# Performance work log

Hardware: AMD Instinct MI355X
Metric: run time of the kernel (lower is better)

The kernel has to match this reference:

```python
import jax, jax.numpy as jnp
import numpy as np

DIM = 768
NUM_HEADS = 1
AGENT_NUM = 4
HEAD_DIM = DIM // NUM_HEADS
SCALE = HEAD_DIM ** -0.5
B, N = 128, 196


def setup_inputs() -> dict:
    key = jax.random.key(0)
    ks = jax.random.split(key, 12)
    s = 0.02
    return {
        "x": jax.random.normal(ks[0], (B, N, DIM), jnp.float32),
        "attn_1": jax.random.normal(ks[1], (B, NUM_HEADS, AGENT_NUM, N), jnp.float32),
        "attn_2": jax.random.normal(ks[2], (B, NUM_HEADS, AGENT_NUM, N), jnp.float32),
        "agent_tk1": jax.random.normal(ks[3], (B, NUM_HEADS, AGENT_NUM, HEAD_DIM), jnp.float32),
        "agent_tk2": jax.random.normal(ks[4], (B, NUM_HEADS, AGENT_NUM, HEAD_DIM), jnp.float32),
        "W_qkv": jax.random.normal(ks[5], (DIM, 3 * DIM), jnp.float32) * s,
        "W_pool1": jax.random.normal(ks[6], (DIM, DIM // 2), jnp.float32) * s,
        "b_pool1": jnp.zeros((DIM // 2,), jnp.float32),
        "W_pool2": jax.random.normal(ks[7], (DIM // 2, NUM_HEADS * AGENT_NUM * DIM), jnp.float32) * s,
        "b_pool2": jnp.zeros((NUM_HEADS * AGENT_NUM * DIM,), jnp.float32),
        "W_proj": jax.random.normal(ks[8], (DIM, DIM), jnp.float32) * s,
        "b_proj": jnp.zeros((DIM,), jnp.float32),
    }


def reference(x, attn_1, attn_2, agent_tk1, agent_tk2,
              W_qkv, W_pool1, b_pool1, W_pool2, b_pool2, W_proj, b_proj):
    b, n, c = x.shape
    # qkv projection: (b, n, 3c) -> q, k, v each (b, n, c)
    qkv = x @ W_qkv
    q, k, v = jnp.split(qkv, 3, axis=-1)

    # agent tokens via pooling MLP on q (exact-erf GELU like torch nn.GELU)
    pooled = jax.nn.gelu(q @ W_pool1 + b_pool1, approximate=False) @ W_pool2 + b_pool2
    # mean over tokens -> (b, num_heads*agent_num*dim) == (b, agent_num*dim) since num_heads==1
    agent_tokens = pooled.mean(axis=1).reshape(b, AGENT_NUM, NUM_HEADS, HEAD_DIM)
    agent_tokens = agent_tokens.transpose(0, 2, 1, 3)  # (b, h, a, d)

    # split heads: (b, h, n, d)
    q = q.reshape(b, n, NUM_HEADS, HEAD_DIM).transpose(0, 2, 1, 3)
    k = k.reshape(b, n, NUM_HEADS, HEAD_DIM).transpose(0, 2, 1, 3)
    v = v.reshape(b, n, NUM_HEADS, HEAD_DIM).transpose(0, 2, 1, 3)

    # stage 1: agent attends to keys -> (b, h, a, n)
    agent_attn = jax.nn.softmax(jnp.einsum("bhad,bhnd->bhan", agent_tokens * SCALE, k), axis=-1)
    agent_rep = agent_attn

    # softmax blending with externally provided attn maps
    s = attn_1 + attn_2
    agent_attn = (agent_attn * jax.nn.softmax(s, axis=-1)
                  + agent_attn * jax.nn.softmax(s, axis=1)
                  + agent_attn) / 3.0

    agent_v = jnp.einsum("bhan,bhnd->bhad", agent_attn, v)  # (b, h, a, d)

    # blend agent tokens with external agent tokens
    t = agent_tk1 + agent_tk2
    agent_tokens = (agent_tokens * jax.nn.softmax(t, axis=-1)
                    + agent_tokens * jax.nn.softmax(t, axis=1)
                    + agent_tokens) / 3.0

    # stage 2: queries attend to agents -> (b, h, n, a)
    q_attn = jax.nn.softmax(jnp.einsum("bhnd,bhad->bhna", q * SCALE, agent_tokens), axis=-1)
    out = jnp.einsum("bhna,bhad->bhnd", q_attn, agent_v)  # (b, h, n, d)

    out = out.transpose(0, 2, 1, 3).reshape(b, n, c)
    out = out @ W_proj + b_proj
    return (out, agent_rep, agent_tokens)
```

## Files before the change

### kernel.cpp

```cpp
#include <hip/hip_runtime.h>
#include <hip/hip_bf16.h>
#include <math.h>

#define NB    128
#define NTOK  196
#define DIMC  768
#define AGN   4
#define SCALE_F 0.036084391824351614f

typedef __bf16  bf16x8  __attribute__((ext_vector_type(8)));
typedef float   f32x4   __attribute__((ext_vector_type(4)));
typedef unsigned short ushortx8 __attribute__((ext_vector_type(8)));
typedef unsigned short ushortx4 __attribute__((ext_vector_type(4)));

__device__ __forceinline__ unsigned short f2bf(float f) {
    union { float f; unsigned int u; } v; v.f = f;
    unsigned int r = v.u + 0x7fffu + ((v.u >> 16) & 1u);
    return (unsigned short)(r >> 16);
}
__device__ __forceinline__ float bf2f(unsigned short u) {
    union { unsigned int u; float f; } v; v.u = ((unsigned int)u) << 16;
    return v.f;
}
__device__ __forceinline__ void load_lds16(const void* g, void* l) {
    __builtin_amdgcn_global_load_lds(
        (const __attribute__((address_space(1))) unsigned int*)g,
        (__attribute__((address_space(3))) unsigned int*)l, 16, 0, 0);
}

template<int EPI>
__global__ __launch_bounds__(256) void gemm_bf16_k(
    const unsigned short* __restrict__ A, int lda,
    const unsigned short* __restrict__ Bt, int ldb,
    const float* __restrict__ bias,
    float* __restrict__ Cf, unsigned short* __restrict__ Cbf,
    int ldc, int K)
{
    __shared__ alignas(16) char lds[16384];

    const int nwg = gridDim.x * gridDim.y;
    const int id  = blockIdx.y * gridDim.x + blockIdx.x;
    const int q8  = nwg >> 3, r8 = nwg & 7;
    const int xcd = id & 7, off = id >> 3;
    const int nid = (xcd < r8 ? xcd * (q8 + 1) : r8 * (q8 + 1) + (xcd - r8) * q8) + off;
    const int bx = nid % gridDim.x, by = nid / gridDim.x;

    const int tid  = threadIdx.x;
    const int lane = tid & 63;
    const int wv   = tid >> 6;
    const int wr   = wv >> 1, wc = wv & 1;
    const int row0 = by * 128;
    const int col0 = bx * 128;

    const int c0 = wv * 2, c1 = wv * 2 + 1;
    const int srow = lane >> 2;
    const int skel = (lane & 3) << 3;
    const unsigned short* Ag0 = A  + (size_t)(row0 + c0*16 + srow) * lda + skel;
    const unsigned short* Ag1 = A  + (size_t)(row0 + c1*16 + srow) * lda + skel;
    const unsigned short* Bg0 = Bt + (size_t)(col0 + c0*16 + srow) * ldb + skel;
    const unsigned short* Bg1 = Bt + (size_t)(col0 + c1*16 + srow) * ldb + skel;
    char* lA0 = lds + c0 * 1024;
    char* lA1 = lds + c1 * 1024;
    char* lB0 = lds + 8192 + c0 * 1024;
    char* lB1 = lds + 8192 + c1 * 1024;

    f32x4 acc[4][4];
    #pragma unroll
    for (int m = 0; m < 4; m++)
        #pragma unroll
        for (int n = 0; n < 4; n++) acc[m][n] = (f32x4){0.f, 0.f, 0.f, 0.f};

    const int frow = lane & 15;
    const int kgrp = (lane >> 4) * 16;

    for (int bk = 0; bk < K; bk += 32) {
        __syncthreads();
        load_lds16(Ag0 + bk, lA0);
        load_lds16(Ag1 + bk, lA1);
        load_lds16(Bg0 + bk, lB0);
        load_lds16(Bg1 + bk, lB1);
        __syncthreads();

        bf16x8 af[4], bf[4];
        #pragma unroll
        for (int m = 0; m < 4; m++)
            af[m] = *(const bf16x8*)(lds + ((wr*64 + m*16 + frow) * 64 + kgrp));
        #pragma unroll
        for (int n = 0; n < 4; n++)
            bf[n] = *(const bf16x8*)(lds + 8192 + ((wc*64 + n*16 + frow) * 64 + kgrp));
        #pragma unroll
        for (int m = 0; m < 4; m++)
            #pragma unroll
            for (int n = 0; n < 4; n++)
                acc[m][n] = __builtin_amdgcn_mfma_f32_16x16x32_bf16(af[m], bf[n], acc[m][n], 0, 0, 0);
    }

    const int crow = (lane >> 4) << 2;
    #pragma unroll
    for (int n = 0; n < 4; n++) {
        const int col = col0 + wc*64 + n*16 + frow;
        const float bn = (EPI > 0) ? bias[col] : 0.f;
        #pragma unroll
        for (int m = 0; m < 4; m++) {
            #pragma unroll
            for (int r = 0; r < 4; r++) {
                const int row = row0 + wr*64 + m*16 + crow + r;
                float v = acc[m][n][r];
                if (EPI > 0) v += bn;
                if (EPI == 2) v = 0.5f * v * (1.f + erff(v * 0.7071067811865476f));
                if (EPI == 0) Cbf[(size_t)row * ldc + col] = f2bf(v);
                else          Cf [(size_t)row * ldc + col] = v;
            }
        }
    }
}

__global__ __launch_bounds__(256) void conv_k(const float* __restrict__ in,
                                              unsigned short* __restrict__ out)
{
    const size_t i = ((size_t)blockIdx.x * 256 + threadIdx.x) * 8;
    float4 v0 = *(const float4*)(in + i);
    float4 v1 = *(const float4*)(in + i + 4);
    ushortx8 o;
    o[0]=f2bf(v0.x); o[1]=f2bf(v0.y); o[2]=f2bf(v0.z); o[3]=f2bf(v0.w);
    o[4]=f2bf(v1.x); o[5]=f2bf(v1.y); o[6]=f2bf(v1.z); o[7]=f2bf(v1.w);
    *(ushortx8*)(out + i) = o;
}

__global__ __launch_bounds__(256) void tconv_k(const float* __restrict__ W,
                                               unsigned short* __restrict__ Wt,
                                               int K, int N)
{
    __shared__ float t[32][33];
    const int n0 = blockIdx.x * 32, k0 = blockIdx.y * 32;
    const int r = threadIdx.x >> 3;
    const int c = (threadIdx.x & 7) * 4;
    float4 v = *(const float4*)&W[(size_t)(k0 + r) * N + n0 + c];
    t[r][c] = v.x; t[r][c+1] = v.y; t[r][c+2] = v.z; t[r][c+3] = v.w;
    __syncthreads();
    ushortx4 o;
    o[0] = f2bf(t[c+0][r]); o[1] = f2bf(t[c+1][r]);
    o[2] = f2bf(t[c+2][r]); o[3] = f2bf(t[c+3][r]);
    *(ushortx4*)&Wt[(size_t)(n0 + r) * K + k0 + c] = o;
}

__global__ __launch_bounds__(128) void mean_k(const float* __restrict__ h1,
                                              float* __restrict__ mh)
{
    const int b = blockIdx.x;
    const int j = blockIdx.y * 128 + threadIdx.x;
    const float* p = h1 + (size_t)b * NTOK * 384 + j;
    float s0 = 0.f, s1 = 0.f, s2 = 0.f, s3 = 0.f;
    for (int n = 0; n < 196; n += 4) {
        s0 += p[(size_t)(n+0) * 384];
        s1 += p[(size_t)(n+1) * 384];
        s2 += p[(size_t)(n+2) * 384];
        s3 += p[(size_t)(n+3) * 384];
    }
    mh[b * 384 + j] = (s0 + s1 + s2 + s3) * (1.f / 196.f);
}

__global__ __launch_bounds__(256) void pool2_k(const float* __restrict__ mh,
                                               const float* __restrict__ W2,
                                               const float* __restrict__ b2,
                                               float* __restrict__ ab)
{
    __shared__ float rows[8][384];
    const int tid = threadIdx.x;
    const int bb0 = blockIdx.y * 8;
    for (int i = tid; i < 8 * 384; i += 256)
        rows[i / 384][i % 384] = mh[(size_t)(bb0 + i / 384) * 384 + (i % 384)];
    __syncthreads();

    const int j = blockIdx.x * 256 + tid;
    const float bj = b2[j];
    float acc[8];
    #pragma unroll
    for (int r = 0; r < 8; r++) acc[r] = bj;
    #pragma unroll 4
    for (int k = 0; k < 384; k++) {
        float w = W2[(size_t)k * 3072 + j];
        #pragma unroll
        for (int r = 0; r < 8; r++) acc[r] = fmaf(rows[r][k], w, acc[r]);
    }
    #pragma unroll
    for (int r = 0; r < 8; r++) ab[(size_t)(bb0 + r) * 3072 + j] = acc[r];
}

__device__ __forceinline__ float wred_max(float v) {
    #pragma unroll
    for (int o = 32; o; o >>= 1) v = fmaxf(v, __shfl_xor(v, o, 64));
    return v;
}
__device__ __forceinline__ float wred_sum(float v) {
    #pragma unroll
    for (int o = 32; o; o >>= 1) v += __shfl_xor(v, o, 64);
    return v;
}

__global__ __launch_bounds__(256) void stage1_k(
    const unsigned short* __restrict__ qkv, const float* __restrict__ agent_base,
    const float* __restrict__ attn1, const float* __restrict__ attn2,
    const float* __restrict__ tk1, const float* __restrict__ tk2,
    unsigned short* __restrict__ agent_v_bf, float* __restrict__ at_blend,
    float* __restrict__ out_rep, float* __restrict__ out_at)
{
    __shared__ float at_s[AGN * DIMC];
    __shared__ float sc[AGN][NTOK];
    __shared__ float s2[AGN][NTOK];

    const int b = blockIdx.x, tid = threadIdx.x;
    for (int i = tid; i < AGN * DIMC; i += 256) at_s[i] = agent_base[(size_t)b * 3072 + i];
    __syncthreads();

    for (int tt = tid; tt < NTOK * 4; tt += 256) {
        const int tok = tt >> 2, qo = tt & 3;
        const unsigned short* krow = qkv + (size_t)(b * NTOK + tok) * 2304 + 768 + qo * 192;
        float s[4] = {0.f, 0.f, 0.f, 0.f};
        for (int d = 0; d < 192; d += 8) {
            ushortx8 kv = *(const ushortx8*)(krow + d);
            float kf[8];
            #pragma unroll
            for (int e = 0; e < 8; e++) kf[e] = bf2f(kv[e]);
            #pragma unroll
            for (int a = 0; a < 4; a++) {
                const float* ap = at_s + a * DIMC + qo * 192 + d;
                float t = 0.f;
                #pragma unroll
                for (int e = 0; e < 8; e++) t = fmaf(ap[e], kf[e], t);
                s[a] += t;
            }
        }
        #pragma unroll
        for (int o = 1; o <= 2; o <<= 1)
            #pragma unroll
            for (int a = 0; a < 4; a++) s[a] += __shfl_xor(s[a], o, 64);
        sc[qo][tok] = s[qo] * SCALE_F;
        s2[qo][tok] = attn1[(size_t)(b*AGN + qo)*NTOK + tok] + attn2[(size_t)(b*AGN + qo)*NTOK + tok];
    }
    __syncthreads();

    const int w = tid >> 6, l = tid & 63;
    {
        const int a = w;
        float m = -1e30f;
        for (int i = l; i < NTOK; i += 64) m = fmaxf(m, sc[a][i]);
        m = wred_max(m);
        float ss = 0.f;
        for (int i = l; i < NTOK; i += 64) { float e = expf(sc[a][i] - m); sc[a][i] = e; ss += e; }
        ss = wred_sum(ss);
        float inv = 1.f / ss;
        for (int i = l; i < NTOK; i += 64) {
            float p = sc[a][i] * inv;
            sc[a][i] = p;
            out_rep[(size_t)(b*AGN + a)*NTOK + i] = p;
        }
        float m2 = -1e30f;
        for (int i = l; i < NTOK; i += 64) m2 = fmaxf(m2, s2[a][i]);
        m2 = wred_max(m2);
        float ss2 = 0.f;
        for (int i = l; i < NTOK; i += 64) { float e = expf(s2[a][i] - m2); s2[a][i] = e; ss2 += e; }
        ss2 = wred_sum(ss2);
        float inv2 = 1.f / ss2;
        for (int i = l; i < NTOK; i += 64)
            s2[a][i] = sc[a][i] * (s2[a][i] * inv2 + 2.f) * (1.f / 3.f);
    }
    __syncthreads();

    for (int d = tid; d < DIMC; d += 256) {
        float av[AGN] = {0.f, 0.f, 0.f, 0.f};
        const unsigned short* vcol = qkv + (size_t)b * NTOK * 2304 + 1536 + d;
        for (int n = 0; n < NTOK; n++) {
            float vv = bf2f(vcol[(size_t)n * 2304]);
            #pragma unroll
            for (int a = 0; a < AGN; a++) av[a] = fmaf(s2[a][n], vv, av[a]);
        }
        #pragma unroll
        for (int a = 0; a < AGN; a++)
            agent_v_bf[(size_t)(b*AGN + a)*DIMC + d] = f2bf(av[a]);
    }

    {
        const int a = w;
        float tv[12];
        float m = -1e30f;
        #pragma unroll
        for (int i = 0; i < 12; i++) {
            int d = l + i * 64;
            tv[i] = tk1[(size_t)(b*AGN + a)*DIMC + d] + tk2[(size_t)(b*AGN + a)*DIMC + d];
            m = fmaxf(m, tv[i]);
        }
        m = wred_max(m);
        float ss = 0.f;
        #pragma unroll
        for (int i = 0; i < 12; i++) { tv[i] = expf(tv[i] - m); ss += tv[i]; }
        ss = wred_sum(ss);
        float inv = 1.f / ss;
        #pragma unroll
        for (int i = 0; i < 12; i++) {
            int d = l + i * 64;
            float ab = at_s[a*DIMC + d] * (tv[i] * inv + 2.f) * (1.f / 3.f);
            at_blend[(size_t)(b*AGN + a)*DIMC + d] = ab;
            out_at[(size_t)(b*AGN + a)*DIMC + d] = ab;
        }
    }
}

__global__ __launch_bounds__(256) void stage2_k(
    const unsigned short* __restrict__ qkv, const float* __restrict__ at_blend,
    const float* __restrict__ avw, float* __restrict__ out)
{
    __shared__ float atb[AGN * DIMC];
    __shared__ float aw[AGN * DIMC];
    __shared__ float qa[49][AGN];

    const int b = blockIdx.y, chunk = blockIdx.x, tid = threadIdx.x;
    for (int i = tid; i < AGN * DIMC; i += 256) {
        atb[i] = at_blend[(size_t)b * 3072 + i];
        aw[i]  = avw[(size_t)b * 3072 + i];
    }
    __syncthreads();

    if (tid < 196) {
        const int tl = tid >> 2;
        const int qo = tid & 3;
        const int tok = chunk * 49 + tl;
        const unsigned short* qrow = qkv + (size_t)(b * NTOK + tok) * 2304 + qo * 192;
        float s[4] = {0.f, 0.f, 0.f, 0.f};
        for (int d = 0; d < 192; d += 8) {
            ushortx8 qv = *(const ushortx8*)(qrow + d);
            float qf[8];
            #pragma unroll
            for (int e = 0; e < 8; e++) qf[e] = bf2f(qv[e]);
            #pragma unroll
            for (int a = 0; a < 4; a++) {
                const float* ap = atb + a * DIMC + qo * 192 + d;
                float t = 0.f;
                #pragma unroll
                for (int e = 0; e < 8; e++) t = fmaf(ap[e], qf[e], t);
                s[a] += t;
            }
        }
        #pragma unroll
        for (int o = 1; o <= 2; o <<= 1)
            #pragma unroll
            for (int a = 0; a < 4; a++) s[a] += __shfl_xor(s[a], o, 64);
        #pragma unroll
        for (int a = 0; a < 4; a++) s[a] *= SCALE_F;
        float m = fmaxf(fmaxf(s[0], s[1]), fmaxf(s[2], s[3]));
        float e[AGN]; float ss = 0.f;
        #pragma unroll
        for (int a = 0; a < 4; a++) { e[a] = expf(s[a] - m); ss += e[a]; }
        qa[tl][qo] = e[qo] / ss;
    }
    __syncthreads();

    for (int nn = 0; nn < 49; nn++) {
        const float p0 = qa[nn][0], p1 = qa[nn][1], p2 = qa[nn][2], p3 = qa[nn][3];
        const size_t rowo = (size_t)(b * NTOK + chunk * 49 + nn) * DIMC;
        for (int d = tid; d < DIMC; d += 256) {
            out[rowo + d] = p0*aw[d] + p1*aw[DIMC + d] + p2*aw[2*DIMC + d] + p3*aw[3*DIMC + d];
        }
    }
}

extern "C" void kernel_launch(void* const* d_in, const int* in_sizes, int n_in,
                              void* d_out, int out_size, void* d_ws, size_t ws_size,
                              hipStream_t stream)
{
    const float* x     = (const float*)d_in[0];
    const float* attn1 = (const float*)d_in[1];
    const float* attn2 = (const float*)d_in[2];
    const float* tk1   = (const float*)d_in[3];
    const float* tk2   = (const float*)d_in[4];
    const float* Wqkv  = (const float*)d_in[5];
    const float* Wp1   = (const float*)d_in[6];
    const float* bp1   = (const float*)d_in[7];
    const float* Wp2   = (const float*)d_in[8];
    const float* bp2   = (const float*)d_in[9];
    const float* Wproj = (const float*)d_in[10];
    const float* bproj = (const float*)d_in[11];

    float* out     = (float*)d_out;
    float* out_rep = out + (size_t)NB * NTOK * DIMC;
    float* out_at  = out_rep + (size_t)NB * AGN * NTOK;

    char* ws = (char*)d_ws;
    unsigned short* qkvbf = (unsigned short*)ws;
    ws += (size_t)NB * NTOK * 2304 * 2;
    unsigned short* xbf = (unsigned short*)ws;
    ws += (size_t)NB * NTOK * DIMC * 2;
    float* h1 = (float*)ws;
    ws += (size_t)NB * NTOK * 384 * 4;
    unsigned short* Wqkvt = (unsigned short*)ws;  ws += (size_t)2304 * 768 * 2;
    unsigned short* Wp1t  = (unsigned short*)ws;  ws += (size_t)384 * 768 * 2;
    unsigned short* Wprojt= (unsigned short*)ws;  ws += (size_t)768 * 768 * 2;
    float* meanh1     = (float*)ws;  ws += (size_t)NB * 384 * 4;
    float* agent_base = (float*)ws;  ws += (size_t)NB * 3072 * 4;
    float* at_blend   = (float*)ws;  ws += (size_t)NB * 3072 * 4;
    unsigned short* agent_v_bf = (unsigned short*)ws;  ws += (size_t)NB * AGN * DIMC * 2;
    float* AVW        = (float*)ws;  ws += (size_t)NB * AGN * DIMC * 4;

    dim3 blk(256);

    conv_k<<<dim3(9408), blk, 0, stream>>>(x, xbf);
    tconv_k<<<dim3(2304/32, 768/32), blk, 0, stream>>>(Wqkv, Wqkvt, 768, 2304);
    tconv_k<<<dim3(384/32, 768/32), blk, 0, stream>>>(Wp1, Wp1t, 768, 384);
    tconv_k<<<dim3(768/32, 768/32), blk, 0, stream>>>(Wproj, Wprojt, 768, 768);

    gemm_bf16_k<0><<<dim3(18, 196), blk, 0, stream>>>(xbf, DIMC, Wqkvt, DIMC,
                                                      nullptr, nullptr, qkvbf, 2304, DIMC);
    gemm_bf16_k<2><<<dim3(3, 196), blk, 0, stream>>>(qkvbf, 2304, Wp1t, DIMC,
                                                     bp1, h1, nullptr, 384, DIMC);
    mean_k<<<dim3(NB, 3), dim3(128), 0, stream>>>(h1, meanh1);
    pool2_k<<<dim3(12, 16), blk, 0, stream>>>(meanh1, Wp2, bp2, agent_base);
    stage1_k<<<dim3(NB), blk, 0, stream>>>(qkvbf, agent_base, attn1, attn2, tk1, tk2,
                                           agent_v_bf, at_blend, out_rep, out_at);
    gemm_bf16_k<1><<<dim3(6, 4), blk, 0, stream>>>(agent_v_bf, DIMC, Wprojt, DIMC,
                                                   bproj, AVW, nullptr, DIMC, DIMC);
    stage2_k<<<dim3(4, NB), blk, 0, stream>>>(qkvbf, at_blend, AVW, out);
}
```

Before: 494.9 us.

## Split agent_v reduction across token chunks and widen stage2 grid

Moves the agent_v weighted sum over tokens out of the per-batch stage1 kernel, which ran only 128 blocks, into a new kernel over 7 token chunks per batch. Its partial sums are combined by a separate reduction kernel that also converts them to bf16. Stage2 is regridded from 4 to 7 chunks per batch to raise occupancy. This adds two launches and an fp32 partial buffer round-trip in exchange for far more parallel blocks on the serial V reduction.

After: 494.4 us. Within noise of the previous version (-0.1%).

```diff
diff --git a/kernel.cpp b/kernel.cpp
--- a/kernel.cpp
+++ b/kernel.cpp
@@ -6,6 +6,7 @@
 #define NTOK  196
 #define DIMC  768
 #define AGN   4
+#define NCHUNK 7
 #define SCALE_F 0.036084391824351614f
 
 typedef __bf16  bf16x8  __attribute__((ext_vector_type(8)));
@@ -198,11 +199,11 @@
     return v;
 }
 
-__global__ __launch_bounds__(256) void stage1_k(
+__global__ __launch_bounds__(256) void s1a_k(
     const unsigned short* __restrict__ qkv, const float* __restrict__ agent_base,
     const float* __restrict__ attn1, const float* __restrict__ attn2,
     const float* __restrict__ tk1, const float* __restrict__ tk2,
-    unsigned short* __restrict__ agent_v_bf, float* __restrict__ at_blend,
+    float* __restrict__ pblend, float* __restrict__ at_blend,
     float* __restrict__ out_rep, float* __restrict__ out_at)
 {
     __shared__ float at_s[AGN * DIMC];
@@ -263,21 +264,8 @@
         ss2 = wred_sum(ss2);
         float inv2 = 1.f / ss2;
         for (int i = l; i < NTOK; i += 64)
-            s2[a][i] = sc[a][i] * (s2[a][i] * inv2 + 2.f) * (1.f / 3.f);
-    }
-    __syncthreads();
-
-    for (int d = tid; d < DIMC; d += 256) {
-        float av[AGN] = {0.f, 0.f, 0.f, 0.f};
-        const unsigned short* vcol = qkv + (size_t)b * NTOK * 2304 + 1536 + d;
-        for (int n = 0; n < NTOK; n++) {
-            float vv = bf2f(vcol[(size_t)n * 2304]);
-            #pragma unroll
-            for (int a = 0; a < AGN; a++) av[a] = fmaf(s2[a][n], vv, av[a]);
-        }
-        #pragma unroll
-        for (int a = 0; a < AGN; a++)
-            agent_v_bf[(size_t)(b*AGN + a)*DIMC + d] = f2bf(av[a]);
+            pblend[(size_t)(b*AGN + a)*NTOK + i] =
+                sc[a][i] * (s2[a][i] * inv2 + 2.f) * (1.f / 3.f);
     }
 
     {
@@ -306,13 +294,60 @@
     }
 }
 
+__global__ __launch_bounds__(256) void s1b_k(
+    const unsigned short* __restrict__ qkv, const float* __restrict__ pblend,
+    float* __restrict__ avpart)
+{
+    __shared__ float pb[AGN][28];
+    const int j = blockIdx.x, b = blockIdx.y, tid = threadIdx.x;
+    const int n0 = j * 28;
+    if (tid < AGN * 28) {
+        const int a = tid / 28, nn = tid % 28;
+        pb[a][nn] = pblend[((size_t)b*AGN + a)*NTOK + n0 + nn];
+    }
+    __syncthreads();
+
+    const unsigned short* vbase = qkv + (size_t)(b * NTOK + n0) * 2304 + 1536;
+    #pragma unroll
+    for (int dd = 0; dd < 3; dd++) {
+        const int d = tid + dd * 256;
+        const unsigned short* vp = vbase + d;
+        float a0 = 0.f, a1 = 0.f, a2 = 0.f, a3 = 0.f;
+        #pragma unroll
+        for (int nn = 0; nn < 28; nn++) {
+            float vv = bf2f(vp[(size_t)nn * 2304]);
+            a0 = fmaf(pb[0][nn], vv, a0);
+            a1 = fmaf(pb[1][nn], vv, a1);
+            a2 = fmaf(pb[2][nn], vv, a2);
+            a3 = fmaf(pb[3][nn], vv, a3);
+        }
+        float* op = avpart + (((size_t)j * NB + b) * AGN) * DIMC + d;
+        op[0*DIMC] = a0; op[1*DIMC] = a1; op[2*DIMC] = a2; op[3*DIMC] = a3;
+    }
+}
+
+__global__ __launch_bounds__(256) void avred_k(const float* __restrict__ avpart,
+                                               unsigned short* __restrict__ avbf)
+{
+    const size_t i = ((size_t)blockIdx.x * 256 + threadIdx.x) * 4;
+    float4 s = *(const float4*)(avpart + i);
+    #pragma unroll
+    for (int j = 1; j < NCHUNK; j++) {
+        float4 t = *(const float4*)(avpart + (size_t)j * NB * AGN * DIMC + i);
+        s.x += t.x; s.y += t.y; s.z += t.z; s.w += t.w;
+    }
+    ushortx4 o;
+    o[0] = f2bf(s.x); o[1] = f2bf(s.y); o[2] = f2bf(s.z); o[3] = f2bf(s.w);
+    *(ushortx4*)(avbf + i) = o;
+}
+
 __global__ __launch_bounds__(256) void stage2_k(
     const unsigned short* __restrict__ qkv, const float* __restrict__ at_blend,
     const float* __restrict__ avw, float* __restrict__ out)
 {
     __shared__ float atb[AGN * DIMC];
     __shared__ float aw[AGN * DIMC];
-    __shared__ float qa[49][AGN];
+    __shared__ float qa[28][AGN];
 
     const int b = blockIdx.y, chunk = blockIdx.x, tid = threadIdx.x;
     for (int i = tid; i < AGN * DIMC; i += 256) {
@@ -321,10 +356,10 @@
     }
     __syncthreads();
 
-    if (tid < 196) {
+    if (tid < 112) {
         const int tl = tid >> 2;
         const int qo = tid & 3;
-        const int tok = chunk * 49 + tl;
+        const int tok = chunk * 28 + tl;
         const unsigned short* qrow = qkv + (size_t)(b * NTOK + tok) * 2304 + qo * 192;
         float s[4] = {0.f, 0.f, 0.f, 0.f};
         for (int d = 0; d < 192; d += 8) {
@@ -355,9 +390,9 @@
     }
     __syncthreads();
 
-    for (int nn = 0; nn < 49; nn++) {
+    for (int nn = 0; nn < 28; nn++) {
         const float p0 = qa[nn][0], p1 = qa[nn][1], p2 = qa[nn][2], p3 = qa[nn][3];
-        const size_t rowo = (size_t)(b * NTOK + chunk * 49 + nn) * DIMC;
+        const size_t rowo = (size_t)(b * NTOK + chunk * 28 + nn) * DIMC;
         for (int d = tid; d < DIMC; d += 256) {
             out[rowo + d] = p0*aw[d] + p1*aw[DIMC + d] + p2*aw[2*DIMC + d] + p3*aw[3*DIMC + d];
         }
@@ -398,6 +433,8 @@
     float* meanh1     = (float*)ws;  ws += (size_t)NB * 384 * 4;
     float* agent_base = (float*)ws;  ws += (size_t)NB * 3072 * 4;
     float* at_blend   = (float*)ws;  ws += (size_t)NB * 3072 * 4;
+    float* pblend     = (float*)ws;  ws += (size_t)NB * AGN * NTOK * 4;
+    float* avpart     = (float*)ws;  ws += (size_t)NCHUNK * NB * AGN * DIMC * 4;
     unsigned short* agent_v_bf = (unsigned short*)ws;  ws += (size_t)NB * AGN * DIMC * 2;
     float* AVW        = (float*)ws;  ws += (size_t)NB * AGN * DIMC * 4;
 
@@ -414,9 +451,11 @@
                                                      bp1, h1, nullptr, 384, DIMC);
     mean_k<<<dim3(NB, 3), dim3(128), 0, stream>>>(h1, meanh1);
     pool2_k<<<dim3(12, 16), blk, 0, stream>>>(meanh1, Wp2, bp2, agent_base);
-    stage1_k<<<dim3(NB), blk, 0, stream>>>(qkvbf, agent_base, attn1, attn2, tk1, tk2,
-                                           agent_v_bf, at_blend, out_rep, out_at);
+    s1a_k<<<dim3(NB), blk, 0, stream>>>(qkvbf, agent_base, attn1, attn2, tk1, tk2,
+                                        pblend, at_blend, out_rep, out_at);
+    s1b_k<<<dim3(NCHUNK, NB), blk, 0, stream>>>(qkvbf, pblend, avpart);
+    avred_k<<<dim3(384), blk, 0, stream>>>(avpart, agent_v_bf);
     gemm_bf16_k<1><<<dim3(6, 4), blk, 0, stream>>>(agent_v_bf, DIMC, Wprojt, DIMC,
                                                    bproj, AVW, nullptr, DIMC, DIMC);
-    stage2_k<<<dim3(4, NB), blk, 0, stream>>>(qkvbf, at_blend, AVW, out);
-}
+    stage2_k<<<dim3(NCHUNK, NB), blk, 0, stream>>>(qkvbf, at_blend, AVW, out);
+}
```
